# Kernel tuning notes

Measured on AMD Instinct MI355X. Metric: run time of the kernel, lower is better.

The kernel has to match this reference:

```python
import jax, jax.numpy as jnp
import numpy as np
import math

# ---------------- static setup: real Clebsch-Gordan coefficients up to L=4 ----------------
L_MAX = 4
DIM = (L_MAX + 1) ** 2  # 25 irrep components
NUM_RADIAL = 64
R_CUT = 5.0
_DEG_OF = np.repeat(np.arange(L_MAX + 1), 2 * np.arange(L_MAX + 1) + 1)  # degree of each lm slot


def _cg_complex(l1, m1, l2, m2, l3, m3):
    if m1 + m2 != m3 or l3 < abs(l1 - l2) or l3 > l1 + l2:
        return 0.0
    f = math.factorial
    pref = math.sqrt((2 * l3 + 1) * f(l1 + l2 - l3) * f(l1 - l2 + l3) * f(-l1 + l2 + l3) / f(l1 + l2 + l3 + 1))
    pref *= math.sqrt(f(l1 + m1) * f(l1 - m1) * f(l2 + m2) * f(l2 - m2) * f(l3 + m3) * f(l3 - m3))
    s = 0.0
    for k in range(l1 + l2 - l3 + 1):
        d = (k, l1 + l2 - l3 - k, l1 - m1 - k, l2 + m2 - k, l3 - l2 + m1 + k, l3 - l1 - m2 + k)
        if min(d) < 0:
            continue
        den = 1
        for x in d:
            den *= f(x)
        s += (-1.0) ** k / den
    return pref * s


def _u_mat(l):
    # complex -> real spherical harmonics change of basis
    U = np.zeros((2 * l + 1, 2 * l + 1), dtype=np.complex128)
    U[l, l] = 1.0
    rs2 = 1.0 / math.sqrt(2.0)
    for m in range(1, l + 1):
        U[l + m, l + m] = (-1.0) ** m * rs2
        U[l + m, l - m] = rs2
        U[l - m, l - m] = 1j * rs2
        U[l - m, l + m] = -1j * (-1.0) ** m * rs2
    return U


def _real_cg():
    C = np.zeros((DIM, DIM, DIM))
    U = [_u_mat(l) for l in range(L_MAX + 1)]
    for l1 in range(L_MAX + 1):
        for l2 in range(L_MAX + 1):
            for l3 in range(L_MAX + 1):
                cgc = np.zeros((2 * l1 + 1, 2 * l2 + 1, 2 * l3 + 1))
                for m1 in range(-l1, l1 + 1):
                    for m2 in range(-l2, l2 + 1):
                        m3 = m1 + m2
                        if abs(m3) <= l3:
                            cgc[l1 + m1, l2 + m2, l3 + m3] = _cg_complex(l1, m1, l2, m2, l3, m3)
                blk = np.einsum('am,bn,cp,mnp->abc', U[l1], U[l2], U[l3].conj(), cgc.astype(np.complex128))
                blk = blk.real if (l1 + l2 + l3) % 2 == 0 else blk.imag
                C[l1 * l1:l1 * l1 + 2 * l1 + 1, l2 * l2:l2 * l2 + 2 * l2 + 1, l3 * l3:l3 * l3 + 2 * l3 + 1] = blk
    return C

_CG = jnp.asarray(_real_cg(), dtype=jnp.float32)  # [25,25,25]


def real_sh(u):
    # u: [P,3] unit vectors -> [P,25] orthonormal real spherical harmonics, L<=4
    x, y, z = u[:, 0], u[:, 1], u[:, 2]
    x2, y2, z2 = x * x, y * y, z * z
    Y = [jnp.full_like(x, 0.28209479177387814),
         0.4886025119029199 * y, 0.4886025119029199 * z, 0.4886025119029199 * x,
         1.0925484305920792 * x * y, 1.0925484305920792 * y * z,
         0.31539156525252005 * (3.0 * z2 - 1.0),
         1.0925484305920792 * x * z, 0.5462742152960396 * (x2 - y2),
         0.5900435899266435 * y * (3.0 * x2 - y2), 2.890611442640554 * x * y * z,
         0.4570457994644658 * y * (5.0 * z2 - 1.0), 0.3731763325901154 * z * (5.0 * z2 - 3.0),
         0.4570457994644658 * x * (5.0 * z2 - 1.0), 1.445305721320277 * z * (x2 - y2),
         0.5900435899266435 * x * (x2 - 3.0 * y2),
         2.5033429417967046 * x * y * (x2 - y2), 1.7701307697799304 * y * z * (3.0 * x2 - y2),
         0.9461746957575601 * x * y * (7.0 * z2 - 1.0), 0.6690465435572892 * y * z * (7.0 * z2 - 3.0),
         0.10578554691520431 * (35.0 * z2 * z2 - 30.0 * z2 + 3.0),
         0.6690465435572892 * x * z * (7.0 * z2 - 3.0), 0.47308734787878004 * (x2 - y2) * (7.0 * z2 - 1.0),
         1.7701307697799304 * x * z * (x2 - 3.0 * y2),
         0.6258357354491761 * (x2 * x2 - 6.0 * x2 * y2 + y2 * y2)]
    return jnp.stack(Y, axis=-1)


def deg_dense(feat, W, b):
    Wlm = W[_DEG_OF]  # [25,Fin,Fout]
    out = jnp.einsum('plf,lfg->plg', feat, Wlm)
    return out.at[:, 0, :].add(b)


def tensor_product(a, b):
    # channelwise CG coupling: out[p,k,f] = sum_ij CG[i,j,k] a[p,i,f] b[p,j,f]
    out = jnp.zeros_like(a)
    for i in range(DIM):  # fixed structural loop over 25 lm slots, avoids [P,25,25,F] temp
        out = out + a[:, i, None, :] * jnp.einsum('jk,pjf->pkf', _CG[i], b)
    return out


def radial_basis(disp, s_j):
    # species-aware radial basis x spherical harmonics -> [P,25,F]
    r = jnp.sqrt(jnp.sum(disp * disp, axis=-1) + 1e-12)
    Y = real_sh(disp / r[:, None])
    centers = jnp.linspace(0.0, R_CUT, NUM_RADIAL, dtype=disp.dtype)
    delta = R_CUT / (NUM_RADIAL - 1)
    g = jnp.exp(-0.5 / (delta * delta) * (r[:, None] - centers) ** 2)
    env = 0.5 * (jnp.cos(jnp.pi * jnp.clip(r / R_CUT, 0.0, 1.0)) + 1.0)  # smooth cutoff
    radial = g * env[:, None] * s_j  # species-modulated radial channels [P,F]
    return Y[:, :, None] * radial[:, None, :]


def setup_inputs() -> dict:
    key = jax.random.key(0)
    ks = jax.random.split(key, 8)
    num_atoms, num_pairs, F = 2048, 32768, 64
    return {
        'atomic_numbers': jax.random.randint(ks[0], (num_atoms,), 0, 119),
        'neighbour_displacements': jax.random.normal(ks[1], (num_pairs, 3), dtype=jnp.float32),
        'neighbour_indices': jax.random.randint(ks[2], (2, num_pairs), 0, num_atoms),
        'species_embed': jax.random.normal(ks[3], (119, F), dtype=jnp.float32),
        'Wt': jax.random.normal(ks[4], (F, F), dtype=jnp.float32) / 8.0,
        'bt': jnp.zeros((F,), dtype=jnp.float32),
        'W1': jax.random.normal(ks[5], (5, F, F), dtype=jnp.float32) / 8.0,
        'b1': jnp.zeros((F,), dtype=jnp.float32),
        'W2': jax.random.normal(ks[6], (5, F, F), dtype=jnp.float32) / 8.0,
        'b2': jnp.zeros((F,), dtype=jnp.float32),
    }


def reference(atomic_numbers, neighbour_displacements, neighbour_indices, species_embed, Wt, bt, W1, b1, W2, b2):
    idx_i, idx_j = neighbour_indices[0], neighbour_indices[1]
    s_j = species_embed[atomic_numbers[idx_j]]                 # gather Z_j embedding
    y = radial_basis(neighbour_displacements, s_j)             # [P,25,F]
    # TensorDense, applied max_moment-1 = 1 time
    y = tensor_product(deg_dense(y, W1, b1), deg_dense(y, W2, b2))
    # 'emb x basis': l1=0 CG is the identity -> channelwise scaling by scalar embedding of Z_i
    emb_i = species_embed[atomic_numbers[idx_i]] @ Wt + bt
    y = y * emb_i[:, None, :]
    out = jax.ops.segment_sum(y, idx_i, num_segments=atomic_numbers.shape[0])  # scatter-sum to atoms
    # residual: scalar embedding added to the l=0 component
    emb = species_embed[atomic_numbers] @ Wt + bt
    return out.at[:, 0, :].add(emb)
```

## Files before the change

### kernel.cpp

```cpp
#include <hip/hip_runtime.h>

#define DEVINL __device__ __forceinline__

typedef __attribute__((ext_vector_type(8))) short bf16x8;
typedef __attribute__((ext_vector_type(8))) unsigned short u16x8;
typedef __attribute__((ext_vector_type(4))) float f32x4;

constexpr int BUCKET = 96;

constexpr int LMAX = 4;

struct Triples { int n; int l1[80], l2[80], l3[80]; };
constexpr Triples make_triples() {
  Triples T{}; T.n = 0;
  for (int a = 0; a <= LMAX; ++a)
    for (int b = 0; b <= LMAX; ++b)
      for (int c = 0; c <= LMAX; ++c) {
        int lo = a > b ? a - b : b - a;
        if (c < lo || c > a + b) continue;
        T.l1[T.n] = a; T.l2[T.n] = b; T.l3[T.n] = c; ++T.n;
      }
  return T;
}
constexpr Triples TRI = make_triples();
static_assert(TRI.n == 65, "triples");

struct ETriT { int n; signed char l1[48], l2[48], l3[48]; };
constexpr ETriT make_etri() {
  ETriT E{}; E.n = 0;
  for (int t = 0; t < TRI.n; ++t)
    if (((TRI.l1[t] + TRI.l2[t] + TRI.l3[t]) & 1) == 0) {
      E.l1[E.n] = (signed char)TRI.l1[t];
      E.l2[E.n] = (signed char)TRI.l2[t];
      E.l3[E.n] = (signed char)TRI.l3[t];
      ++E.n;
    }
  return E;
}
constexpr ETriT ETRI = make_etri();
static_assert(ETRI.n == 42, "even triples");

constexpr double FT[14] = {1., 1., 2., 6., 24., 120., 720., 5040., 40320.,
                           362880., 3628800., 39916800., 479001600., 6227020800.};

constexpr double csqrt(double x) {
  if (x <= 0.0) return 0.0;
  double y = 1.0;
  while (y * y < x) y *= 2.0;
  for (int i = 0; i < 30; ++i) y = 0.5 * (y + x / y);
  return y;
}

constexpr double cg_complex(int l1, int m1, int l2, int m2, int l3, int m3) {
  if (m1 + m2 != m3) return 0.0;
  double pref = csqrt((2.0 * l3 + 1.0) * FT[l1 + l2 - l3] * FT[l1 - l2 + l3] *
                      FT[-l1 + l2 + l3] / FT[l1 + l2 + l3 + 1]);
  pref *= csqrt(FT[l1 + m1] * FT[l1 - m1] * FT[l2 + m2] * FT[l2 - m2] *
                FT[l3 + m3] * FT[l3 - m3]);
  double s = 0.0;
  for (int k = 0; k <= l1 + l2 - l3; ++k) {
    int d3 = l1 - m1 - k, d4 = l2 + m2 - k, d5 = l3 - l2 + m1 + k, d6 = l3 - l1 - m2 + k;
    if (d3 < 0 || d4 < 0 || d5 < 0 || d6 < 0) continue;
    double den = FT[k] * FT[l1 + l2 - l3 - k] * FT[d3] * FT[d4] * FT[d5] * FT[d6];
    s += ((k & 1) ? -1.0 : 1.0) / den;
  }
  return pref * s;
}

struct CURow { int n; int m[2]; double re[2], im[2]; };
constexpr CURow cu_row(int l, int a) {
  CURow u{}; int ma = a - l;
  const double RS2 = 0.70710678118654752440;
  if (ma == 0) { u.n = 1; u.m[0] = 0; u.re[0] = 1.0; u.im[0] = 0.0; }
  else if (ma > 0) {
    u.n = 2;
    u.m[0] = ma;  u.re[0] = ((ma & 1) ? -RS2 : RS2); u.im[0] = 0.0;
    u.m[1] = -ma; u.re[1] = RS2;                     u.im[1] = 0.0;
  } else {
    int mm = -ma; u.n = 2;
    u.m[0] = -mm; u.re[0] = 0.0; u.im[0] = RS2;
    u.m[1] =  mm; u.re[1] = 0.0; u.im[1] = ((mm & 1) ? RS2 : -RS2);
  }
  return u;
}

constexpr double real_cg_entry(int l1, int a, int l2, int b, int l3, int c) {
  CURow u1 = cu_row(l1, a), u2 = cu_row(l2, b), u3 = cu_row(l3, c);
  double sre = 0.0, sim = 0.0;
  for (int x = 0; x < u1.n; ++x)
    for (int y = 0; y < u2.n; ++y)
      for (int z = 0; z < u3.n; ++z) {
        int m1 = u1.m[x], m2 = u2.m[y], m3 = u3.m[z];
        if (m1 + m2 != m3) continue;
        double cg = cg_complex(l1, m1, l2, m2, l3, m3);
        if (cg == 0.0) continue;
        double are = u1.re[x], aim = u1.im[x], bre = u2.re[y], bim = u2.im[y];
        double pre = are * bre - aim * bim, pim = are * bim + aim * bre;
        double cre = u3.re[z], cim = -u3.im[z];
        sre += (pre * cre - pim * cim) * cg;
        sim += (pre * cim + pim * cre) * cg;
      }
  return ((l1 + l2 + l3) & 1) ? sim : sre;
}

struct Y25D { double y[25]; };
constexpr Y25D csh25(double x, double y, double z) {
  Y25D Y{};
  double x2 = x * x, y2 = y * y, z2 = z * z;
  Y.y[0] = 0.28209479177387814;
  Y.y[1] = 0.4886025119029199 * y;
  Y.y[2] = 0.4886025119029199 * z;
  Y.y[3] = 0.4886025119029199 * x;
  Y.y[4] = 1.0925484305920792 * x * y;
  Y.y[5] = 1.0925484305920792 * y * z;
  Y.y[6] = 0.31539156525252005 * (3.0 * z2 - 1.0);
  Y.y[7] = 1.0925484305920792 * x * z;
  Y.y[8] = 0.5462742152960396 * (x2 - y2);
  Y.y[9] = 0.5900435899266435 * y * (3.0 * x2 - y2);
  Y.y[10] = 2.890611442640554 * x * y * z;
  Y.y[11] = 0.4570457994644658 * y * (5.0 * z2 - 1.0);
  Y.y[12] = 0.3731763325901154 * z * (5.0 * z2 - 3.0);
  Y.y[13] = 0.4570457994644658 * x * (5.0 * z2 - 1.0);
  Y.y[14] = 1.445305721320277 * z * (x2 - y2);
  Y.y[15] = 0.5900435899266435 * x * (x2 - 3.0 * y2);
  Y.y[16] = 2.5033429417967046 * x * y * (x2 - y2);
  Y.y[17] = 1.7701307697799304 * y * z * (3.0 * x2 - y2);
  Y.y[18] = 0.9461746957575601 * x * y * (7.0 * z2 - 1.0);
  Y.y[19] = 0.6690465435572892 * y * z * (7.0 * z2 - 3.0);
  Y.y[20] = 0.10578554691520431 * (35.0 * z2 * z2 - 30.0 * z2 + 3.0);
  Y.y[21] = 0.6690465435572892 * x * z * (7.0 * z2 - 3.0);
  Y.y[22] = 0.47308734787878004 * (x2 - y2) * (7.0 * z2 - 1.0);
  Y.y[23] = 1.7701307697799304 * x * z * (x2 - 3.0 * y2);
  Y.y[24] = 0.6258357354491761 * (x2 * x2 - 6.0 * x2 * y2 + y2 * y2);
  return Y;
}

constexpr double compute_A_even(int e) {
  int l1 = ETRI.l1[e], l2 = ETRI.l2[e], l3 = ETRI.l3[e];
  double ux = 0.437, uy = -0.602, uz = 0.668;
  double n = csqrt(ux * ux + uy * uy + uz * uz);
  Y25D Y = csh25(ux / n, uy / n, uz / n);
  int c0 = 2 * l3;
  double den = Y.y[l3 * l3 + c0];
  double num = 0.0;
  for (int a = 0; a < 2 * l1 + 1; ++a)
    for (int b = 0; b < 2 * l2 + 1; ++b) {
      double v = real_cg_entry(l1, a, l2, b, l3, c0);
      if (v != 0.0) num += v * Y.y[l1 * l1 + a] * Y.y[l2 * l2 + b];
    }
  return num / den;
}

template <int E> inline constexpr float A_of = (float)compute_A_even(E);
constexpr float AT42[42] = {
    A_of<0>,  A_of<1>,  A_of<2>,  A_of<3>,  A_of<4>,  A_of<5>,  A_of<6>,
    A_of<7>,  A_of<8>,  A_of<9>,  A_of<10>, A_of<11>, A_of<12>, A_of<13>,
    A_of<14>, A_of<15>, A_of<16>, A_of<17>, A_of<18>, A_of<19>, A_of<20>,
    A_of<21>, A_of<22>, A_of<23>, A_of<24>, A_of<25>, A_of<26>, A_of<27>,
    A_of<28>, A_of<29>, A_of<30>, A_of<31>, A_of<32>, A_of<33>, A_of<34>,
    A_of<35>, A_of<36>, A_of<37>, A_of<38>, A_of<39>, A_of<40>, A_of<41>};

DEVINL unsigned short f2bf(float x) {
  unsigned u = __float_as_uint(x);
  u += 0x7FFFu + ((u >> 16) & 1u);
  return (unsigned short)(u >> 16);
}
DEVINL float bf2f(unsigned short b) { return __uint_as_float((unsigned)b << 16); }

DEVINL void sh25(float x, float y, float z, float* Y) {
  float x2 = x * x, y2 = y * y, z2 = z * z;
  Y[0] = 0.28209479177387814f;
  Y[1] = 0.4886025119029199f * y;
  Y[2] = 0.4886025119029199f * z;
  Y[3] = 0.4886025119029199f * x;
  Y[4] = 1.0925484305920792f * x * y;
  Y[5] = 1.0925484305920792f * y * z;
  Y[6] = 0.31539156525252005f * (3.0f * z2 - 1.0f);
  Y[7] = 1.0925484305920792f * x * z;
  Y[8] = 0.5462742152960396f * (x2 - y2);
  Y[9] = 0.5900435899266435f * y * (3.0f * x2 - y2);
  Y[10] = 2.890611442640554f * x * y * z;
  Y[11] = 0.4570457994644658f * y * (5.0f * z2 - 1.0f);
  Y[12] = 0.3731763325901154f * z * (5.0f * z2 - 3.0f);
  Y[13] = 0.4570457994644658f * x * (5.0f * z2 - 1.0f);
  Y[14] = 1.445305721320277f * z * (x2 - y2);
  Y[15] = 0.5900435899266435f * x * (x2 - 3.0f * y2);
  Y[16] = 2.5033429417967046f * x * y * (x2 - y2);
  Y[17] = 1.7701307697799304f * y * z * (3.0f * x2 - y2);
  Y[18] = 0.9461746957575601f * x * y * (7.0f * z2 - 1.0f);
  Y[19] = 0.6690465435572892f * y * z * (7.0f * z2 - 3.0f);
  Y[20] = 0.10578554691520431f * (35.0f * z2 * z2 - 30.0f * z2 + 3.0f);
  Y[21] = 0.6690465435572892f * x * z * (7.0f * z2 - 3.0f);
  Y[22] = 0.47308734787878004f * (x2 - y2) * (7.0f * z2 - 1.0f);
  Y[23] = 1.7701307697799304f * x * z * (x2 - 3.0f * y2);
  Y[24] = 0.6258357354491761f * (x2 * x2 - 6.0f * x2 * y2 + y2 * y2);
}

__global__ void ktw(const float* __restrict__ W1, const float* __restrict__ W2,
                    unsigned short* __restrict__ WT, int* __restrict__ counts, int A) {
  int idx = blockIdx.x * 256 + threadIdx.x;
  if (blockIdx.x == 159) {
    for (int i = threadIdx.x; i < A; i += 256) counts[i] = 0;
  }
  if (idx >= 40960) return;
  int c = idx & 63, g = (idx >> 6) & 63, l = idx >> 12;
  const float* W = (l < 5) ? (W1 + (size_t)l * 4096) : (W2 + (size_t)(l - 5) * 4096);
  WT[idx] = f2bf(W[c * 64 + g]);
}

__global__ __launch_bounds__(256) void kA(const int* __restrict__ Z,
                                          const int* __restrict__ nbr,
                                          const float* __restrict__ disp,
                                          const float* __restrict__ se,
                                          const unsigned short* __restrict__ WT,
                                          const float* __restrict__ b1,
                                          const float* __restrict__ b2,
                                          unsigned short* __restrict__ G,
                                          int* __restrict__ counts,
                                          int* __restrict__ plist2,
                                          int P) {
  const int nGemm = (P / 128) * 4;
  const int t = threadIdx.x;

  if ((int)blockIdx.x >= nGemm) {
    int p = ((int)blockIdx.x - nGemm) * 256 + t;
    if (p < P) {
      int a = nbr[p];
      int rank = atomicAdd(&counts[a], 1);
      if (rank < BUCKET) plist2[a * BUCKET + rank] = p;
    }
    return;
  }

  __shared__ alignas(16) unsigned short rad[128 * 72];
  const int bid = blockIdx.x;
  const int p0 = (bid >> 2) * 128;
  const int g0 = (bid & 3) * 16;

  {
    int pl = t >> 1, half = t & 1;
    int p = p0 + pl;
    int zj = Z[nbr[P + p]];
    float dx = disp[3 * p], dy = disp[3 * p + 1], dz = disp[3 * p + 2];
    float r = sqrtf(dx * dx + dy * dy + dz * dz + 1e-12f);
    float env = 0.5f * (__cosf(3.14159265358979f * fminf(r * 0.2f, 1.0f)) + 1.0f);
    const float delta = 5.0f / 63.0f;
    const float w = 0.5f / (delta * delta);
    int c0 = half * 32;
    const float4* s4 = (const float4*)(se + (size_t)zj * 64 + c0);
    unsigned* radw = (unsigned*)rad;
#pragma unroll
    for (int i = 0; i < 8; ++i) {
      float4 s = s4[i];
      float d0 = r - (float)(c0 + 4 * i + 0) * delta;
      float d1 = r - (float)(c0 + 4 * i + 1) * delta;
      float d2 = r - (float)(c0 + 4 * i + 2) * delta;
      float d3 = r - (float)(c0 + 4 * i + 3) * delta;
      float v0 = __expf(-w * d0 * d0) * env * s.x;
      float v1 = __expf(-w * d1 * d1) * env * s.y;
      float v2 = __expf(-w * d2 * d2) * env * s.z;
      float v3 = __expf(-w * d3 * d3) * env * s.w;
      radw[pl * 36 + half * 16 + 2 * i] =
          (unsigned)f2bf(v0) | ((unsigned)f2bf(v1) << 16);
      radw[pl * 36 + half * 16 + 2 * i + 1] =
          (unsigned)f2bf(v2) | ((unsigned)f2bf(v3) << 16);
    }
  }
  __syncthreads();

  const int lane = t & 63, wv = t >> 6;
  const int n = lane & 15, quad = lane >> 4;
  const int g = g0 + n;
  const float invY0 = 3.5449077018110318f;

  bf16x8 B[10][2];
#pragma unroll
  for (int l = 0; l < 10; ++l)
#pragma unroll
    for (int kk = 0; kk < 2; ++kk)
      B[l][kk] = *(const bf16x8*)(WT + (((size_t)l * 64 + g) * 64 + kk * 32 + quad * 8));

  float bb1 = b1[g] * invY0, bb2 = b2[g] * invY0;

  const int m0 = wv * 32;
#pragma unroll
  for (int mt = 0; mt < 2; ++mt) {
    int row = m0 + mt * 16 + n;
    bf16x8 A0 = *(const bf16x8*)(rad + row * 72 + quad * 8);
    bf16x8 A1 = *(const bf16x8*)(rad + row * 72 + 32 + quad * 8);
    f32x4 C[10];
#pragma unroll
    for (int l = 0; l < 10; ++l) C[l] = (f32x4){0.f, 0.f, 0.f, 0.f};
#pragma unroll
    for (int l = 0; l < 10; ++l) {
      C[l] = __builtin_amdgcn_mfma_f32_16x16x32_bf16(A0, B[l][0], C[l], 0, 0, 0);
      C[l] = __builtin_amdgcn_mfma_f32_16x16x32_bf16(A1, B[l][1], C[l], 0, 0, 0);
    }
#pragma unroll
    for (int r = 0; r < 4; ++r) { C[0][r] += bb1; C[5][r] += bb2; }

    f32x4 Gac[5];
#pragma unroll
    for (int l = 0; l < 5; ++l) Gac[l] = (f32x4){0.f, 0.f, 0.f, 0.f};
#pragma unroll
    for (int l1 = 0; l1 < 5; ++l1)
#pragma unroll
      for (int l2 = 0; l2 < 5; ++l2) {
        f32x4 pr = C[l1] * C[5 + l2];
#pragma unroll
        for (int e = 0; e < 42; ++e)
          if ((int)ETRI.l1[e] == l1 && (int)ETRI.l2[e] == l2)
            Gac[(int)ETRI.l3[e]] += AT42[e] * pr;
      }

    int prow = p0 + m0 + mt * 16 + quad * 4;
#pragma unroll
    for (int r = 0; r < 4; ++r) {
      u16x8 pack;
      pack[0] = f2bf(Gac[0][r]); pack[1] = f2bf(Gac[1][r]);
      pack[2] = f2bf(Gac[2][r]); pack[3] = f2bf(Gac[3][r]);
      pack[4] = f2bf(Gac[4][r]); pack[5] = 0; pack[6] = 0; pack[7] = 0;
      *(u16x8*)(G + (size_t)(prow + r) * 512 + g * 8) = pack;
    }
  }
}

__global__ __launch_bounds__(256) void k3(const unsigned short* __restrict__ G,
                                          const float* __restrict__ disp,
                                          const int* __restrict__ Z,
                                          const float* __restrict__ se,
                                          const float* __restrict__ Wt,
                                          const float* __restrict__ bt,
                                          const int* __restrict__ counts,
                                          const int* __restrict__ plist2,
                                          float* __restrict__ out, int P) {
  __shared__ float red[3 * 1600];
  int atom = blockIdx.x;
  int f = threadIdx.x & 63, wv = threadIdx.x >> 6;
  float acc[25];
#pragma unroll
  for (int k = 0; k < 25; ++k) acc[k] = 0.f;
  int cnt = counts[atom];
  cnt = cnt < BUCKET ? cnt : BUCKET;
  const int* bucket = plist2 + (size_t)atom * BUCKET;

  int q = wv;
  u16x8 gv;
  float cdx = 0.f, cdy = 0.f, cdz = 0.f;
  if (q < cnt) {
    int p = __builtin_amdgcn_readfirstlane(bucket[q]);
    gv = *(const u16x8*)(G + (size_t)p * 512 + f * 8);
    cdx = disp[3 * p]; cdy = disp[3 * p + 1]; cdz = disp[3 * p + 2];
  }
  while (q < cnt) {
    u16x8 gcur = gv;
    float dx = cdx, dy = cdy, dz = cdz;
    int qn = q + 4;
    if (qn < cnt) {
      int p = __builtin_amdgcn_readfirstlane(bucket[qn]);
      gv = *(const u16x8*)(G + (size_t)p * 512 + f * 8);
      cdx = disp[3 * p]; cdy = disp[3 * p + 1]; cdz = disp[3 * p + 2];
    }
    float g0 = bf2f(gcur[0]), g1 = bf2f(gcur[1]), g2 = bf2f(gcur[2]);
    float g3 = bf2f(gcur[3]), g4 = bf2f(gcur[4]);
    float r = sqrtf(dx * dx + dy * dy + dz * dz + 1e-12f);
    float inv = 1.0f / r;
    float Y[25];
    sh25(dx * inv, dy * inv, dz * inv, Y);
    acc[0] = fmaf(Y[0], g0, acc[0]);
#pragma unroll
    for (int k = 1; k < 4; ++k)   acc[k] = fmaf(Y[k], g1, acc[k]);
#pragma unroll
    for (int k = 4; k < 9; ++k)   acc[k] = fmaf(Y[k], g2, acc[k]);
#pragma unroll
    for (int k = 9; k < 16; ++k)  acc[k] = fmaf(Y[k], g3, acc[k]);
#pragma unroll
    for (int k = 16; k < 25; ++k) acc[k] = fmaf(Y[k], g4, acc[k]);
    q = qn;
  }

  if (wv > 0) {
#pragma unroll
    for (int k = 0; k < 25; ++k) red[(wv - 1) * 1600 + k * 64 + f] = acc[k];
  }
  __syncthreads();
  if (wv == 0) {
#pragma unroll
    for (int k = 0; k < 25; ++k)
      acc[k] += red[k * 64 + f] + red[1600 + k * 64 + f] + red[3200 + k * 64 + f];
    int z = Z[atom];
    float e = bt[f];
    for (int c = 0; c < 64; ++c)
      e = fmaf(se[(size_t)z * 64 + c], Wt[(size_t)c * 64 + f], e);
#pragma unroll
    for (int k = 0; k < 25; ++k)
      out[(size_t)atom * 1600 + (size_t)k * 64 + f] = fmaf(acc[k], e, (k == 0) ? e : 0.f);
  }
}

static inline size_t align256(size_t x) { return (x + 255) & ~(size_t)255; }

extern "C" void kernel_launch(void* const* d_in, const int* in_sizes, int n_in,
                              void* d_out, int out_size, void* d_ws, size_t ws_size,
                              hipStream_t stream) {
  const int*   Z    = (const int*)d_in[0];
  const float* disp = (const float*)d_in[1];
  const int*   nbr  = (const int*)d_in[2];
  const float* se   = (const float*)d_in[3];
  const float* Wt   = (const float*)d_in[4];
  const float* bt   = (const float*)d_in[5];
  const float* W1   = (const float*)d_in[6];
  const float* b1   = (const float*)d_in[7];
  const float* W2   = (const float*)d_in[8];
  const float* b2   = (const float*)d_in[9];
  float* out = (float*)d_out;

  const int A = in_sizes[0];
  const int P = in_sizes[1] / 3;

  char* ws = (char*)d_ws;
  size_t o = 0;
  unsigned short* G  = (unsigned short*)(ws + o); o += align256((size_t)P * 512 * 2);
  unsigned short* WT = (unsigned short*)(ws + o); o += align256((size_t)40960 * 2);
  int* counts = (int*)(ws + o); o += align256((size_t)A * 4);
  int* plist2 = (int*)(ws + o); o += align256((size_t)A * BUCKET * 4);
  (void)ws_size; (void)n_in; (void)out_size;

  const int nGemm = (P / 128) * 4, nHist = P / 256;

  ktw<<<160, 256, 0, stream>>>(W1, W2, WT, counts, A);
  kA<<<nGemm + nHist, 256, 0, stream>>>(Z, nbr, disp, se, WT, b1, b2, G,
                                        counts, plist2, P);
  k3<<<A, 256, 0, stream>>>(G, disp, Z, se, Wt, bt, counts, plist2, out, P);
}
```

Before: 120.6 us.

## Pack unit directions into G padding and map one atom per wave

kA now handles 64 pairs per block and loops over all four 16-channel chunks, so the radial basis is computed once per pair instead of once per chunk. It also stores the normalized direction as fp16 in the three unused padding slots of each G record. k3 assigns one atom per wave, with four atoms per block, so the shared-memory reduction and barrier are gone. It reads the direction from G, which drops the separate displacement loads and the sqrt/divide. The trade-offs are fp16 rounding of the direction, a serial neighbour loop per wave, and fewer GEMM blocks that each do more work.

```diff
diff --git a/kernel.cpp b/kernel.cpp
--- a/kernel.cpp
+++ b/kernel.cpp
@@ -166,6 +166,12 @@
   return (unsigned short)(u >> 16);
 }
 DEVINL float bf2f(unsigned short b) { return __uint_as_float((unsigned)b << 16); }
+DEVINL unsigned short f2h(float x) {
+  return __builtin_bit_cast(unsigned short, (_Float16)x);
+}
+DEVINL float h2f(unsigned short h) {
+  return (float)__builtin_bit_cast(_Float16, h);
+}
 
 DEVINL void sh25(float x, float y, float z, float* Y) {
   float x2 = x * x, y2 = y * y, z2 = z * z;
@@ -219,7 +225,7 @@
                                           int* __restrict__ counts,
                                           int* __restrict__ plist2,
                                           int P) {
-  const int nGemm = (P / 128) * 4;
+  const int nGemm = P / 64;
   const int t = threadIdx.x;
 
   if ((int)blockIdx.x >= nGemm) {
@@ -232,13 +238,12 @@
     return;
   }
 
-  __shared__ alignas(16) unsigned short rad[128 * 72];
-  const int bid = blockIdx.x;
-  const int p0 = (bid >> 2) * 128;
-  const int g0 = (bid & 3) * 16;
+  __shared__ alignas(16) unsigned short rad[64 * 72];
+  __shared__ unsigned short dird[64 * 3];
+  const int p0 = (int)blockIdx.x * 64;
 
   {
-    int pl = t >> 1, half = t & 1;
+    int pl = t >> 2, qt = t & 3;
     int p = p0 + pl;
     int zj = Z[nbr[P + p]];
     float dx = disp[3 * p], dy = disp[3 * p + 1], dz = disp[3 * p + 2];
@@ -246,11 +251,17 @@
     float env = 0.5f * (__cosf(3.14159265358979f * fminf(r * 0.2f, 1.0f)) + 1.0f);
     const float delta = 5.0f / 63.0f;
     const float w = 0.5f / (delta * delta);
-    int c0 = half * 32;
+    if (qt == 0) {
+      float inv = 1.0f / r;
+      dird[pl * 3 + 0] = f2h(dx * inv);
+      dird[pl * 3 + 1] = f2h(dy * inv);
+      dird[pl * 3 + 2] = f2h(dz * inv);
+    }
+    int c0 = qt * 16;
     const float4* s4 = (const float4*)(se + (size_t)zj * 64 + c0);
     unsigned* radw = (unsigned*)rad;
 #pragma unroll
-    for (int i = 0; i < 8; ++i) {
+    for (int i = 0; i < 4; ++i) {
       float4 s = s4[i];
       float d0 = r - (float)(c0 + 4 * i + 0) * delta;
       float d1 = r - (float)(c0 + 4 * i + 1) * delta;
@@ -260,34 +271,42 @@
       float v1 = __expf(-w * d1 * d1) * env * s.y;
       float v2 = __expf(-w * d2 * d2) * env * s.z;
       float v3 = __expf(-w * d3 * d3) * env * s.w;
-      radw[pl * 36 + half * 16 + 2 * i] =
-          (unsigned)f2bf(v0) | ((unsigned)f2bf(v1) << 16);
-      radw[pl * 36 + half * 16 + 2 * i + 1] =
-          (unsigned)f2bf(v2) | ((unsigned)f2bf(v3) << 16);
+      radw[pl * 36 + qt * 8 + 2 * i]     = (unsigned)f2bf(v0) | ((unsigned)f2bf(v1) << 16);
+      radw[pl * 36 + qt * 8 + 2 * i + 1] = (unsigned)f2bf(v2) | ((unsigned)f2bf(v3) << 16);
     }
   }
   __syncthreads();
 
   const int lane = t & 63, wv = t >> 6;
   const int n = lane & 15, quad = lane >> 4;
-  const int g = g0 + n;
   const float invY0 = 3.5449077018110318f;
 
-  bf16x8 B[10][2];
-#pragma unroll
-  for (int l = 0; l < 10; ++l)
-#pragma unroll
-    for (int kk = 0; kk < 2; ++kk)
-      B[l][kk] = *(const bf16x8*)(WT + (((size_t)l * 64 + g) * 64 + kk * 32 + quad * 8));
-
-  float bb1 = b1[g] * invY0, bb2 = b2[g] * invY0;
-
-  const int m0 = wv * 32;
-#pragma unroll
-  for (int mt = 0; mt < 2; ++mt) {
-    int row = m0 + mt * 16 + n;
-    bf16x8 A0 = *(const bf16x8*)(rad + row * 72 + quad * 8);
-    bf16x8 A1 = *(const bf16x8*)(rad + row * 72 + 32 + quad * 8);
+  const int row = wv * 16 + n;
+  bf16x8 A0 = *(const bf16x8*)(rad + row * 72 + quad * 8);
+  bf16x8 A1 = *(const bf16x8*)(rad + row * 72 + 32 + quad * 8);
+
+  unsigned short dh[4][3];
+#pragma unroll
+  for (int r = 0; r < 4; ++r) {
+    int lp = wv * 16 + quad * 4 + r;
+    dh[r][0] = dird[lp * 3 + 0];
+    dh[r][1] = dird[lp * 3 + 1];
+    dh[r][2] = dird[lp * 3 + 2];
+  }
+
+#pragma unroll 1
+  for (int ch = 0; ch < 4; ++ch) {
+    const int g = ch * 16 + n;
+
+    bf16x8 B[10][2];
+#pragma unroll
+    for (int l = 0; l < 10; ++l)
+#pragma unroll
+      for (int kk = 0; kk < 2; ++kk)
+        B[l][kk] = *(const bf16x8*)(WT + (((size_t)l * 64 + g) * 64 + kk * 32 + quad * 8));
+
+    float bb1 = b1[g] * invY0, bb2 = b2[g] * invY0;
+
     f32x4 C[10];
 #pragma unroll
     for (int l = 0; l < 10; ++l) C[l] = (f32x4){0.f, 0.f, 0.f, 0.f};
@@ -313,60 +332,55 @@
             Gac[(int)ETRI.l3[e]] += AT42[e] * pr;
       }
 
-    int prow = p0 + m0 + mt * 16 + quad * 4;
+    const int prow = p0 + wv * 16 + quad * 4;
 #pragma unroll
     for (int r = 0; r < 4; ++r) {
       u16x8 pack;
       pack[0] = f2bf(Gac[0][r]); pack[1] = f2bf(Gac[1][r]);
       pack[2] = f2bf(Gac[2][r]); pack[3] = f2bf(Gac[3][r]);
-      pack[4] = f2bf(Gac[4][r]); pack[5] = 0; pack[6] = 0; pack[7] = 0;
+      pack[4] = f2bf(Gac[4][r]);
+      pack[5] = dh[r][0]; pack[6] = dh[r][1]; pack[7] = dh[r][2];
       *(u16x8*)(G + (size_t)(prow + r) * 512 + g * 8) = pack;
     }
   }
 }
 
 __global__ __launch_bounds__(256) void k3(const unsigned short* __restrict__ G,
-                                          const float* __restrict__ disp,
                                           const int* __restrict__ Z,
                                           const float* __restrict__ se,
                                           const float* __restrict__ Wt,
                                           const float* __restrict__ bt,
                                           const int* __restrict__ counts,
                                           const int* __restrict__ plist2,
-                                          float* __restrict__ out, int P) {
-  __shared__ float red[3 * 1600];
-  int atom = blockIdx.x;
-  int f = threadIdx.x & 63, wv = threadIdx.x >> 6;
+                                          float* __restrict__ out, int A) {
+  const int wv = threadIdx.x >> 6, f = threadIdx.x & 63;
+  const int atom = blockIdx.x * 4 + wv;
+  if (atom >= A) return;
+
   float acc[25];
 #pragma unroll
   for (int k = 0; k < 25; ++k) acc[k] = 0.f;
+
   int cnt = counts[atom];
   cnt = cnt < BUCKET ? cnt : BUCKET;
   const int* bucket = plist2 + (size_t)atom * BUCKET;
 
-  int q = wv;
   u16x8 gv;
-  float cdx = 0.f, cdy = 0.f, cdz = 0.f;
-  if (q < cnt) {
-    int p = __builtin_amdgcn_readfirstlane(bucket[q]);
+  if (cnt > 0) {
+    int p = __builtin_amdgcn_readfirstlane(bucket[0]);
     gv = *(const u16x8*)(G + (size_t)p * 512 + f * 8);
-    cdx = disp[3 * p]; cdy = disp[3 * p + 1]; cdz = disp[3 * p + 2];
-  }
-  while (q < cnt) {
-    u16x8 gcur = gv;
-    float dx = cdx, dy = cdy, dz = cdz;
-    int qn = q + 4;
-    if (qn < cnt) {
-      int p = __builtin_amdgcn_readfirstlane(bucket[qn]);
+  }
+  for (int q = 0; q < cnt; ++q) {
+    u16x8 gc = gv;
+    if (q + 1 < cnt) {
+      int p = __builtin_amdgcn_readfirstlane(bucket[q + 1]);
       gv = *(const u16x8*)(G + (size_t)p * 512 + f * 8);
-      cdx = disp[3 * p]; cdy = disp[3 * p + 1]; cdz = disp[3 * p + 2];
-    }
-    float g0 = bf2f(gcur[0]), g1 = bf2f(gcur[1]), g2 = bf2f(gcur[2]);
-    float g3 = bf2f(gcur[3]), g4 = bf2f(gcur[4]);
-    float r = sqrtf(dx * dx + dy * dy + dz * dz + 1e-12f);
-    float inv = 1.0f / r;
+    }
+    float g0 = bf2f(gc[0]), g1 = bf2f(gc[1]), g2 = bf2f(gc[2]);
+    float g3 = bf2f(gc[3]), g4 = bf2f(gc[4]);
+    float ux = h2f(gc[5]), uy = h2f(gc[6]), uz = h2f(gc[7]);
     float Y[25];
-    sh25(dx * inv, dy * inv, dz * inv, Y);
+    sh25(ux, uy, uz, Y);
     acc[0] = fmaf(Y[0], g0, acc[0]);
 #pragma unroll
     for (int k = 1; k < 4; ++k)   acc[k] = fmaf(Y[k], g1, acc[k]);
@@ -376,26 +390,16 @@
     for (int k = 9; k < 16; ++k)  acc[k] = fmaf(Y[k], g3, acc[k]);
 #pragma unroll
     for (int k = 16; k < 25; ++k) acc[k] = fmaf(Y[k], g4, acc[k]);
-    q = qn;
-  }
-
-  if (wv > 0) {
-#pragma unroll
-    for (int k = 0; k < 25; ++k) red[(wv - 1) * 1600 + k * 64 + f] = acc[k];
-  }
-  __syncthreads();
-  if (wv == 0) {
-#pragma unroll
-    for (int k = 0; k < 25; ++k)
-      acc[k] += red[k * 64 + f] + red[1600 + k * 64 + f] + red[3200 + k * 64 + f];
-    int z = Z[atom];
-    float e = bt[f];
-    for (int c = 0; c < 64; ++c)
-      e = fmaf(se[(size_t)z * 64 + c], Wt[(size_t)c * 64 + f], e);
-#pragma unroll
-    for (int k = 0; k < 25; ++k)
-      out[(size_t)atom * 1600 + (size_t)k * 64 + f] = fmaf(acc[k], e, (k == 0) ? e : 0.f);
-  }
+  }
+
+  int z = Z[atom];
+  float e = bt[f];
+  for (int c = 0; c < 64; ++c)
+    e = fmaf(se[(size_t)z * 64 + c], Wt[(size_t)c * 64 + f], e);
+
+#pragma unroll
+  for (int k = 0; k < 25; ++k)
+    out[(size_t)atom * 1600 + (size_t)k * 64 + f] = fmaf(acc[k], e, (k == 0) ? e : 0.f);
 }
 
 static inline size_t align256(size_t x) { return (x + 255) & ~(size_t)255; }
@@ -426,10 +430,10 @@
   int* plist2 = (int*)(ws + o); o += align256((size_t)A * BUCKET * 4);
   (void)ws_size; (void)n_in; (void)out_size;
 
-  const int nGemm = (P / 128) * 4, nHist = P / 256;
+  const int nGemm = P / 64, nHist = P / 256;
 
   ktw<<<160, 256, 0, stream>>>(W1, W2, WT, counts, A);
   kA<<<nGemm + nHist, 256, 0, stream>>>(Z, nbr, disp, se, WT, b1, b2, G,
                                         counts, plist2, P);
-  k3<<<A, 256, 0, stream>>>(G, disp, Z, se, Wt, bt, counts, plist2, out, P);
-}
+  k3<<<(A + 3) / 4, 256, 0, stream>>>(G, Z, se, Wt, bt, counts, plist2, out, A);
+}
```

After: 125.5 us. 4.1% more time.

## Pack fp16 unit directions into G padding and process two atoms per block

Applied to the files above, without the earlier changes.

The GEMM kernel now stores each pair's normalized direction as fp16 in the three unused padding slots of every G row. The scatter kernel therefore no longer reads displacements or computes sqrt and reciprocal per pair. The scatter kernel also handles two atoms per block with two waves each, preloads bucket indices once and broadcasts them by shuffle, and keeps three G loads in flight. The trade-offs are lower direction precision in fp16 and less intra-atom parallelism per atom.

```diff
diff --git a/kernel.cpp b/kernel.cpp
--- a/kernel.cpp
+++ b/kernel.cpp
@@ -166,6 +166,12 @@
   return (unsigned short)(u >> 16);
 }
 DEVINL float bf2f(unsigned short b) { return __uint_as_float((unsigned)b << 16); }
+DEVINL unsigned short f2h(float x) {
+  return __builtin_bit_cast(unsigned short, (_Float16)x);
+}
+DEVINL float h2f(unsigned short h) {
+  return (float)__builtin_bit_cast(_Float16, h);
+}
 
 DEVINL void sh25(float x, float y, float z, float* Y) {
   float x2 = x * x, y2 = y * y, z2 = z * z;
@@ -233,6 +239,7 @@
   }
 
   __shared__ alignas(16) unsigned short rad[128 * 72];
+  __shared__ unsigned short dird[128 * 3];
   const int bid = blockIdx.x;
   const int p0 = (bid >> 2) * 128;
   const int g0 = (bid & 3) * 16;
@@ -246,6 +253,12 @@
     float env = 0.5f * (__cosf(3.14159265358979f * fminf(r * 0.2f, 1.0f)) + 1.0f);
     const float delta = 5.0f / 63.0f;
     const float w = 0.5f / (delta * delta);
+    if (half == 0) {
+      float inv = 1.0f / r;
+      dird[pl * 3 + 0] = f2h(dx * inv);
+      dird[pl * 3 + 1] = f2h(dy * inv);
+      dird[pl * 3 + 2] = f2h(dz * inv);
+    }
     int c0 = half * 32;
     const float4* s4 = (const float4*)(se + (size_t)zj * 64 + c0);
     unsigned* radw = (unsigned*)rad;
@@ -313,81 +326,102 @@
             Gac[(int)ETRI.l3[e]] += AT42[e] * pr;
       }
 
-    int prow = p0 + m0 + mt * 16 + quad * 4;
+    const int lrow = m0 + mt * 16 + quad * 4;
 #pragma unroll
     for (int r = 0; r < 4; ++r) {
       u16x8 pack;
       pack[0] = f2bf(Gac[0][r]); pack[1] = f2bf(Gac[1][r]);
       pack[2] = f2bf(Gac[2][r]); pack[3] = f2bf(Gac[3][r]);
-      pack[4] = f2bf(Gac[4][r]); pack[5] = 0; pack[6] = 0; pack[7] = 0;
-      *(u16x8*)(G + (size_t)(prow + r) * 512 + g * 8) = pack;
+      pack[4] = f2bf(Gac[4][r]);
+      pack[5] = dird[(lrow + r) * 3 + 0];
+      pack[6] = dird[(lrow + r) * 3 + 1];
+      pack[7] = dird[(lrow + r) * 3 + 2];
+      *(u16x8*)(G + (size_t)(p0 + lrow + r) * 512 + g * 8) = pack;
     }
   }
 }
 
 __global__ __launch_bounds__(256) void k3(const unsigned short* __restrict__ G,
-                                          const float* __restrict__ disp,
                                           const int* __restrict__ Z,
                                           const float* __restrict__ se,
                                           const float* __restrict__ Wt,
                                           const float* __restrict__ bt,
                                           const int* __restrict__ counts,
                                           const int* __restrict__ plist2,
-                                          float* __restrict__ out, int P) {
-  __shared__ float red[3 * 1600];
-  int atom = blockIdx.x;
-  int f = threadIdx.x & 63, wv = threadIdx.x >> 6;
+                                          float* __restrict__ out, int A) {
+  __shared__ float red[2 * 1600];
+  const int wv = threadIdx.x >> 6, f = threadIdx.x & 63;
+  const int la = wv >> 1;
+  const int h = wv & 1;
+  const int atom = blockIdx.x * 2 + la;
+  const int atomc = atom < A ? atom : A - 1;
+
   float acc[25];
 #pragma unroll
   for (int k = 0; k < 25; ++k) acc[k] = 0.f;
-  int cnt = counts[atom];
+
+  int cnt = (atom < A) ? counts[atomc] : 0;
   cnt = cnt < BUCKET ? cnt : BUCKET;
-  const int* bucket = plist2 + (size_t)atom * BUCKET;
-
-  int q = wv;
-  u16x8 gv;
-  float cdx = 0.f, cdy = 0.f, cdz = 0.f;
-  if (q < cnt) {
-    int p = __builtin_amdgcn_readfirstlane(bucket[q]);
-    gv = *(const u16x8*)(G + (size_t)p * 512 + f * 8);
-    cdx = disp[3 * p]; cdy = disp[3 * p + 1]; cdz = disp[3 * p + 2];
-  }
-  while (q < cnt) {
-    u16x8 gcur = gv;
-    float dx = cdx, dy = cdy, dz = cdz;
-    int qn = q + 4;
-    if (qn < cnt) {
-      int p = __builtin_amdgcn_readfirstlane(bucket[qn]);
-      gv = *(const u16x8*)(G + (size_t)p * 512 + f * 8);
-      cdx = disp[3 * p]; cdy = disp[3 * p + 1]; cdz = disp[3 * p + 2];
-    }
-    float g0 = bf2f(gcur[0]), g1 = bf2f(gcur[1]), g2 = bf2f(gcur[2]);
-    float g3 = bf2f(gcur[3]), g4 = bf2f(gcur[4]);
-    float r = sqrtf(dx * dx + dy * dy + dz * dz + 1e-12f);
-    float inv = 1.0f / r;
-    float Y[25];
-    sh25(dx * inv, dy * inv, dz * inv, Y);
-    acc[0] = fmaf(Y[0], g0, acc[0]);
-#pragma unroll
-    for (int k = 1; k < 4; ++k)   acc[k] = fmaf(Y[k], g1, acc[k]);
-#pragma unroll
-    for (int k = 4; k < 9; ++k)   acc[k] = fmaf(Y[k], g2, acc[k]);
-#pragma unroll
-    for (int k = 9; k < 16; ++k)  acc[k] = fmaf(Y[k], g3, acc[k]);
-#pragma unroll
-    for (int k = 16; k < 25; ++k) acc[k] = fmaf(Y[k], g4, acc[k]);
-    q = qn;
-  }
-
-  if (wv > 0) {
-#pragma unroll
-    for (int k = 0; k < 25; ++k) red[(wv - 1) * 1600 + k * 64 + f] = acc[k];
+  const int* bucket = plist2 + (size_t)atomc * BUCKET;
+  int rb0 = bucket[f];
+  int rb1 = bucket[64 + (f & 31)];
+
+  int nq = (cnt > h) ? ((cnt - h + 1) >> 1) : 0;
+
+#define GETP(i)                                                     \
+  ({ int q_ = h + 2 * (i);                                          \
+     (q_ < 64) ? __shfl(rb0, q_) : __shfl(rb1, q_ - 64); })
+#define LDG(p_) (*(const u16x8*)(G + (size_t)(p_)*512 + f * 8))
+
+  u16x8 v0, v1, v2;
+  if (nq > 0) v0 = LDG(GETP(0));
+  if (nq > 1) v1 = LDG(GETP(1));
+  if (nq > 2) v2 = LDG(GETP(2));
+
+#define BODY(gc)                                                    \
+  {                                                                 \
+    float g0 = bf2f(gc[0]), g1 = bf2f(gc[1]), g2 = bf2f(gc[2]);     \
+    float g3 = bf2f(gc[3]), g4 = bf2f(gc[4]);                       \
+    float ux = h2f(gc[5]), uy = h2f(gc[6]), uz = h2f(gc[7]);        \
+    float Y[25];                                                    \
+    sh25(ux, uy, uz, Y);                                            \
+    acc[0] = fmaf(Y[0], g0, acc[0]);                                \
+    _Pragma("unroll") for (int k = 1; k < 4; ++k)                   \
+        acc[k] = fmaf(Y[k], g1, acc[k]);                            \
+    _Pragma("unroll") for (int k = 4; k < 9; ++k)                   \
+        acc[k] = fmaf(Y[k], g2, acc[k]);                            \
+    _Pragma("unroll") for (int k = 9; k < 16; ++k)                  \
+        acc[k] = fmaf(Y[k], g3, acc[k]);                            \
+    _Pragma("unroll") for (int k = 16; k < 25; ++k)                 \
+        acc[k] = fmaf(Y[k], g4, acc[k]);                            \
+  }
+
+  int i = 0;
+  while (i < nq) {
+    BODY(v0);
+    if (i + 3 < nq) v0 = LDG(GETP(i + 3));
+    ++i;
+    if (i >= nq) break;
+    BODY(v1);
+    if (i + 3 < nq) v1 = LDG(GETP(i + 3));
+    ++i;
+    if (i >= nq) break;
+    BODY(v2);
+    if (i + 3 < nq) v2 = LDG(GETP(i + 3));
+    ++i;
+  }
+#undef BODY
+#undef LDG
+#undef GETP
+
+  if (h == 1) {
+#pragma unroll
+    for (int k = 0; k < 25; ++k) red[la * 1600 + k * 64 + f] = acc[k];
   }
   __syncthreads();
-  if (wv == 0) {
-#pragma unroll
-    for (int k = 0; k < 25; ++k)
-      acc[k] += red[k * 64 + f] + red[1600 + k * 64 + f] + red[3200 + k * 64 + f];
+  if (h == 0 && atom < A) {
+#pragma unroll
+    for (int k = 0; k < 25; ++k) acc[k] += red[la * 1600 + k * 64 + f];
     int z = Z[atom];
     float e = bt[f];
     for (int c = 0; c < 64; ++c)
@@ -431,5 +465,5 @@
   ktw<<<160, 256, 0, stream>>>(W1, W2, WT, counts, A);
   kA<<<nGemm + nHist, 256, 0, stream>>>(Z, nbr, disp, se, WT, b1, b2, G,
                                         counts, plist2, P);
-  k3<<<A, 256, 0, stream>>>(G, disp, Z, se, Wt, bt, counts, plist2, out, P);
-}
+  k3<<<(A + 1) / 2, 256, 0, stream>>>(G, Z, se, Wt, bt, counts, plist2, out, A);
+}
```

After: 121.0 us. About the same (+0.4%).
